# Kernel tuning notes

Hardware: AMD Instinct MI355X
Metric: run time of the kernel (lower is better)

Reference implementation:

```python
import jax, jax.numpy as jnp
import numpy as np

D_MODEL = 1024
N_HEADS = 16
D_K = D_MODEL // N_HEADS  # 64


def setup_inputs() -> dict:
    key = jax.random.key(0)
    ks = jax.random.split(key, 12)
    B, S = 2, 2048
    inp = {
        "query": jax.random.normal(ks[0], (B, S, D_MODEL), jnp.float32),
        "key": jax.random.normal(ks[1], (B, S, D_MODEL), jnp.float32),
        "value": jax.random.normal(ks[2], (B, S, D_MODEL), jnp.float32),
        "mask": jnp.ones((B, 1, S, S), jnp.int32),
    }
    sc = 1.0 / np.sqrt(D_MODEL)
    inp["Wq"] = jax.random.normal(ks[3], (D_MODEL, D_MODEL), jnp.float32) * sc
    inp["bq"] = jnp.zeros((D_MODEL,), jnp.float32)
    inp["Wk"] = jax.random.normal(ks[4], (D_MODEL, D_MODEL), jnp.float32) * sc
    inp["bk"] = jnp.zeros((D_MODEL,), jnp.float32)
    inp["Wv"] = jax.random.normal(ks[5], (D_MODEL, D_MODEL), jnp.float32) * sc
    inp["bv"] = jnp.zeros((D_MODEL,), jnp.float32)
    inp["Wo"] = jax.random.normal(ks[6], (D_MODEL, D_MODEL), jnp.float32) * sc
    inp["bo"] = jnp.zeros((D_MODEL,), jnp.float32)
    return inp


def reference(query, key, value, mask, Wq, bq, Wk, bk, Wv, bv, Wo, bo):
    B, Sq, _ = query.shape
    H, dk = N_HEADS, D_K
    # linear projections, split heads: (B,S,D) -> (B,H,S,dk)
    def split_heads(x):
        return x.reshape(B, -1, H, dk).transpose(0, 2, 1, 3)
    Q = split_heads(query @ Wq.T + bq)
    K = split_heads(key @ Wk.T + bk)
    V = split_heads(value @ Wv.T + bv)
    scale = 1.0 / jnp.sqrt(jnp.asarray(dk, jnp.float32))
    scores = jnp.einsum('bhqd,bhkd->bhqk', Q, K) * scale
    scores = jnp.where(mask == 0, jnp.asarray(-1e9, scores.dtype), scores)
    attn = jax.nn.softmax(scores, axis=-1)  # (B,H,Sq,Sk)
    out = jnp.einsum('bhqk,bhkd->bhqd', attn, V)
    out = out.transpose(0, 2, 1, 3).reshape(B, Sq, D_MODEL)
    out = out @ Wo.T + bo
    return out, attn
```

## Files before the change

kernel.cpp:

```cpp
#include <hip/hip_runtime.h>
#include <cstdint>
#include <cstddef>

#define DEV __device__ __forceinline__

typedef float f32x4 __attribute__((ext_vector_type(4)));
typedef __bf16 bf16x8 __attribute__((ext_vector_type(8)));
typedef unsigned short u16x8 __attribute__((ext_vector_type(8)));

static constexpr int D = 1024, H = 16, DK = 64, S = 2048, B = 2;
static constexpr int M_TOT = B * S;
static constexpr size_t OUT0 = (size_t)M_TOT * D;

DEV unsigned short f2bf(float f) {
  unsigned x = __builtin_bit_cast(unsigned, f);
  unsigned r = (x + 0x7fffu + ((x >> 16) & 1u)) >> 16;
  return (unsigned short)r;
}

DEV float bf2f(unsigned short u) {
  return __builtin_bit_cast(float, (unsigned)u << 16);
}

DEV f32x4 mfma_bf16(bf16x8 a, bf16x8 b, f32x4 c) {
  return __builtin_amdgcn_mfma_f32_16x16x32_bf16(a, b, c, 0, 0, 0);
}

DEV bf16x8 bc(u16x8 u) { return __builtin_bit_cast(bf16x8, u); }

template <int MODE, bool ABF16, bool WBF16>
DEV void proj_body(unsigned short* As, unsigned short* Bs, const void* Aptr,
                   const void* W, const float* bias, void* dst) {
  constexpr int BM = 128, BK = 32, LDT = 40;
  const int tid = threadIdx.x;
  const int lane = tid & 63, wave = tid >> 6;
  const int wrow = wave >> 1, wcol = wave & 1;
  const int l15 = lane & 15, kg = lane >> 4;
  const int m0 = blockIdx.y * BM, n0 = blockIdx.x * BM;
  const int srow = tid >> 1, scb = (tid & 1) * 16;

  f32x4 acc[4][4] = {};

  for (int kt = 0; kt < D; kt += BK) {
    {
      u16x8 t0, t1;
      if constexpr (ABF16) {
        const unsigned short* ap =
            (const unsigned short*)Aptr + (size_t)(m0 + srow) * D + kt + scb;
        t0 = *(const u16x8*)ap;
        t1 = *(const u16x8*)(ap + 8);
      } else {
        const float* ap = (const float*)Aptr + (size_t)(m0 + srow) * D + kt + scb;
        float4 v0 = *(const float4*)(ap + 0);
        float4 v1 = *(const float4*)(ap + 4);
        float4 v2 = *(const float4*)(ap + 8);
        float4 v3 = *(const float4*)(ap + 12);
        t0[0] = f2bf(v0.x); t0[1] = f2bf(v0.y); t0[2] = f2bf(v0.z); t0[3] = f2bf(v0.w);
        t0[4] = f2bf(v1.x); t0[5] = f2bf(v1.y); t0[6] = f2bf(v1.z); t0[7] = f2bf(v1.w);
        t1[0] = f2bf(v2.x); t1[1] = f2bf(v2.y); t1[2] = f2bf(v2.z); t1[3] = f2bf(v2.w);
        t1[4] = f2bf(v3.x); t1[5] = f2bf(v3.y); t1[6] = f2bf(v3.z); t1[7] = f2bf(v3.w);
      }
      *(u16x8*)&As[srow * LDT + scb] = t0;
      *(u16x8*)&As[srow * LDT + scb + 8] = t1;

      u16x8 s0, s1;
      if constexpr (WBF16) {
        const unsigned short* wp =
            (const unsigned short*)W + (size_t)(n0 + srow) * D + kt + scb;
        s0 = *(const u16x8*)wp;
        s1 = *(const u16x8*)(wp + 8);
      } else {
        const float* bp = (const float*)W + (size_t)(n0 + srow) * D + kt + scb;
        float4 w0 = *(const float4*)(bp + 0);
        float4 w1 = *(const float4*)(bp + 4);
        float4 w2 = *(const float4*)(bp + 8);
        float4 w3 = *(const float4*)(bp + 12);
        s0[0] = f2bf(w0.x); s0[1] = f2bf(w0.y); s0[2] = f2bf(w0.z); s0[3] = f2bf(w0.w);
        s0[4] = f2bf(w1.x); s0[5] = f2bf(w1.y); s0[6] = f2bf(w1.z); s0[7] = f2bf(w1.w);
        s1[0] = f2bf(w2.x); s1[1] = f2bf(w2.y); s1[2] = f2bf(w2.z); s1[3] = f2bf(w2.w);
        s1[4] = f2bf(w3.x); s1[5] = f2bf(w3.y); s1[6] = f2bf(w3.z); s1[7] = f2bf(w3.w);
      }
      *(u16x8*)&Bs[srow * LDT + scb] = s0;
      *(u16x8*)&Bs[srow * LDT + scb + 8] = s1;
    }
    __syncthreads();

    bf16x8 a[4], b[4];
#pragma unroll
    for (int i = 0; i < 4; i++)
      a[i] = bc(*(const u16x8*)&As[(wrow * 64 + i * 16 + l15) * LDT + kg * 8]);
#pragma unroll
    for (int i = 0; i < 4; i++)
      b[i] = bc(*(const u16x8*)&Bs[(wcol * 64 + i * 16 + l15) * LDT + kg * 8]);
#pragma unroll
    for (int mi = 0; mi < 4; mi++)
#pragma unroll
      for (int ni = 0; ni < 4; ni++) acc[mi][ni] = mfma_bf16(a[mi], b[ni], acc[mi][ni]);
    __syncthreads();
  }

#pragma unroll
  for (int mi = 0; mi < 4; mi++) {
#pragma unroll
    for (int ni = 0; ni < 4; ni++) {
      const int n = n0 + wcol * 64 + ni * 16 + l15;
      const float bval = bias[n];
#pragma unroll
      for (int r = 0; r < 4; r++) {
        const int m = m0 + wrow * 64 + mi * 16 + kg * 4 + r;
        float v = acc[mi][ni][r] + bval;
        if constexpr (MODE == 0) v *= 0.125f;
        if constexpr (MODE == 0 || MODE == 1) {
          const int b_ = m >> 11, s = m & (S - 1), h = n >> 6, d_ = n & (DK - 1);
          ((unsigned short*)dst)[(((size_t)(b_ * H + h)) * S + s) * DK + d_] = f2bf(v);
        } else if constexpr (MODE == 2) {
          const int b_ = m >> 11, s = m & (S - 1), h = n >> 6, d_ = n & (DK - 1);
          ((unsigned short*)dst)[(((size_t)(b_ * H + h)) * DK + d_) * S + s] = f2bf(v);
        } else {
          ((float*)dst)[(size_t)m * D + n] = v;
        }
      }
    }
  }
}

struct PrepArgs {
  const float* A[3];
  const float* W[3];
  const float* bias[3];
  unsigned short* dst[3];
  const int* mask;
  unsigned long long* bits;
  const float* Wo;
  unsigned short* WoBf;
};

__global__ __launch_bounds__(256) void qkv_prep(PrepArgs pa) {
  __shared__ __align__(16) unsigned short As[128 * 40];
  __shared__ __align__(16) unsigned short Bs[128 * 40];
  const int z = blockIdx.z;
  if (z == 0) {
    proj_body<0, false, false>(As, Bs, pa.A[0], pa.W[0], pa.bias[0], pa.dst[0]);
  } else if (z == 1) {
    proj_body<1, false, false>(As, Bs, pa.A[1], pa.W[1], pa.bias[1], pa.dst[1]);
  } else if (z == 2) {
    proj_body<2, false, false>(As, Bs, pa.A[2], pa.W[2], pa.bias[2], pa.dst[2]);
  } else {
    const int gid = blockIdx.y * 8 + blockIdx.x;
    const int tid = threadIdx.x, lane = tid & 63;
    const int base = gid * 512;
    for (int w = base + (tid >> 6); w < base + 512; w += 4) {
      int m = __builtin_nontemporal_load(pa.mask + (size_t)w * 64 + lane);
      unsigned long long bal = __ballot(m != 0);
      if (lane == 0) pa.bits[w] = bal;
    }
    {
      const size_t i0 = (size_t)gid * 4096 + (size_t)tid * 16;
      float4 v0 = *(const float4*)(pa.Wo + i0);
      float4 v1 = *(const float4*)(pa.Wo + i0 + 4);
      float4 v2 = *(const float4*)(pa.Wo + i0 + 8);
      float4 v3 = *(const float4*)(pa.Wo + i0 + 12);
      u16x8 t0, t1;
      t0[0] = f2bf(v0.x); t0[1] = f2bf(v0.y); t0[2] = f2bf(v0.z); t0[3] = f2bf(v0.w);
      t0[4] = f2bf(v1.x); t0[5] = f2bf(v1.y); t0[6] = f2bf(v1.z); t0[7] = f2bf(v1.w);
      t1[0] = f2bf(v2.x); t1[1] = f2bf(v2.y); t1[2] = f2bf(v2.z); t1[3] = f2bf(v2.w);
      t1[4] = f2bf(v3.x); t1[5] = f2bf(v3.y); t1[6] = f2bf(v3.z); t1[7] = f2bf(v3.w);
      *(u16x8*)(pa.WoBf + i0) = t0;
      *(u16x8*)(pa.WoBf + i0 + 8) = t1;
    }
  }
}

__global__ __launch_bounds__(256) void out_proj(const unsigned short* __restrict__ ctx,
                                                const unsigned short* __restrict__ WoBf,
                                                const float* __restrict__ bo,
                                                float* __restrict__ out) {
  __shared__ __align__(16) unsigned short As[128 * 40];
  __shared__ __align__(16) unsigned short Bs[128 * 40];
  proj_body<3, true, true>(As, Bs, ctx, WoBf, bo, out);
}

__global__ __launch_bounds__(1024, 4) void attn_kernel(
    const unsigned short* __restrict__ Qb, const unsigned short* __restrict__ Kb,
    const unsigned short* __restrict__ Vt, const unsigned* __restrict__ bits32,
    float* __restrict__ attn_out, unsigned short* __restrict__ ctx) {
  constexpr int QB = 32, SROW = 2056;
  __shared__ __align__(16) unsigned short es[QB * SROW];
  __shared__ unsigned mlds[QB * 64];
  __shared__ float rsum[16 * QB];
  __shared__ float rinv_s[QB];
  __shared__ float opart[4 * QB * 17];

  const int wg = blockIdx.x;
  const int qblk = wg & 63, h = (wg >> 6) & 15, b_ = wg >> 10;
  const int bh = b_ * H + h;
  const int qb0 = qblk * QB;
  const int tid = threadIdx.x, lane = tid & 63, wave = tid >> 6;
  const int l15 = lane & 15, kg = lane >> 4;
  const int rowq = kg * 4;
  constexpr float LOG2E = 1.44269504088896340736f;

#pragma unroll
  for (int i = 0; i < 2; i++) {
    const int idx = tid + i * 1024;
    mlds[idx] = bits32[((size_t)b_ * S + qb0 + (idx >> 6)) * 64 + (idx & 63)];
  }

  const unsigned short* qbase = Qb + ((size_t)bh * S + qb0) * DK;
  bf16x8 aq[2][2];
#pragma unroll
  for (int rg = 0; rg < 2; rg++)
#pragma unroll
    for (int hf = 0; hf < 2; hf++)
      aq[rg][hf] =
          bc(*(const u16x8*)(qbase + (size_t)(rg * 16 + l15) * DK + hf * 32 + kg * 8));
  __syncthreads();

  float sum[2][4] = {};
#pragma unroll 2
  for (int i = 0; i < 8; i++) {
    const int t = wave * 8 + i;
    const unsigned short* krow = Kb + ((size_t)bh * S + t * 16 + l15) * DK;
    bf16x8 b0 = bc(*(const u16x8*)(krow + kg * 8));
    bf16x8 b1 = bc(*(const u16x8*)(krow + 32 + kg * 8));
    const unsigned shift = (unsigned)((t & 1) * 16 + l15);
#pragma unroll
    for (int rg = 0; rg < 2; rg++) {
      f32x4 c = {0.f, 0.f, 0.f, 0.f};
      c = mfma_bf16(aq[rg][0], b0, c);
      c = mfma_bf16(aq[rg][1], b1, c);
#pragma unroll
      for (int r = 0; r < 4; r++) {
        const int row = rg * 16 + rowq + r;
        const unsigned w = mlds[row * 64 + (t >> 1)];
        const float e = ((w >> shift) & 1u) ? exp2f(c[r] * LOG2E) : 0.f;
        sum[rg][r] += e;
        es[row * SROW + t * 16 + l15] = f2bf(e);
      }
    }
  }

#pragma unroll
  for (int rg = 0; rg < 2; rg++)
#pragma unroll
    for (int r = 0; r < 4; r++) {
      float s = sum[rg][r];
      s += __shfl_xor(s, 1);
      s += __shfl_xor(s, 2);
      s += __shfl_xor(s, 4);
      s += __shfl_xor(s, 8);
      if (l15 == 0) rsum[wave * QB + rg * 16 + rowq + r] = s;
    }
  __syncthreads();
  if (tid < QB) {
    float t2 = 0.f;
#pragma unroll
    for (int w = 0; w < 16; w++) t2 += rsum[w * QB + tid];
    rinv_s[tid] = 1.f / t2;
  }
  __syncthreads();

  f32x4 o[2] = {};
  if (wave < 8) {
#pragma unroll
    for (int rr = 0; rr < 4; rr++) {
      const int row = wave * 4 + rr;
      const float ri = rinv_s[row];
      float* dstp = attn_out + ((size_t)bh * S + qb0 + row) * S;
#pragma unroll
      for (int j = 0; j < 4; j++) {
        u16x8 u = *(const u16x8*)&es[row * SROW + j * 512 + lane * 8];
        f32x4 lo, hi;
        lo[0] = bf2f(u[0]) * ri; lo[1] = bf2f(u[1]) * ri;
        lo[2] = bf2f(u[2]) * ri; lo[3] = bf2f(u[3]) * ri;
        hi[0] = bf2f(u[4]) * ri; hi[1] = bf2f(u[5]) * ri;
        hi[2] = bf2f(u[6]) * ri; hi[3] = bf2f(u[7]) * ri;
        __builtin_nontemporal_store(lo, (f32x4*)(dstp + j * 512 + lane * 8));
        __builtin_nontemporal_store(hi, (f32x4*)(dstp + j * 512 + lane * 8 + 4));
      }
    }
  } else {
    const int pw = wave - 8, dg = pw & 3, kh = pw >> 2;
    const unsigned short* vrow =
        Vt + ((size_t)bh * DK + dg * 16 + l15) * S + kh * 1024;
    const unsigned short* ebase = es + kh * 1024 + kg * 8;
#pragma unroll 2
    for (int ks = 0; ks < 32; ks++) {
      bf16x8 bv = bc(*(const u16x8*)(vrow + ks * 32 + kg * 8));
#pragma unroll
      for (int rg = 0; rg < 2; rg++) {
        bf16x8 af = bc(*(const u16x8*)&ebase[(size_t)(rg * 16 + l15) * SROW + ks * 32]);
        o[rg] = mfma_bf16(af, bv, o[rg]);
      }
    }
    if (kh == 1) {
#pragma unroll
      for (int rg = 0; rg < 2; rg++)
#pragma unroll
        for (int r = 0; r < 4; r++)
          opart[dg * (QB * 17) + (rg * 16 + rowq + r) * 17 + l15] = o[rg][r];
    }
  }
  __syncthreads();

  if (wave >= 8 && ((wave - 8) >> 2) == 0) {
    const int dg = (wave - 8) & 3;
#pragma unroll
    for (int rg = 0; rg < 2; rg++)
#pragma unroll
      for (int r = 0; r < 4; r++) {
        const int row = rg * 16 + rowq + r;
        const float v =
            (o[rg][r] + opart[dg * (QB * 17) + row * 17 + l15]) * rinv_s[row];
        ctx[((size_t)(b_ * S + qb0 + row)) * D + h * DK + dg * 16 + l15] = f2bf(v);
      }
  }
}

extern "C" void kernel_launch(void* const* d_in, const int* in_sizes, int n_in,
                              void* d_out, int out_size, void* d_ws, size_t ws_size,
                              hipStream_t stream) {
  const float* query = (const float*)d_in[0];
  const float* key   = (const float*)d_in[1];
  const float* value = (const float*)d_in[2];
  const int*   mask  = (const int*)d_in[3];
  const float* Wq = (const float*)d_in[4];
  const float* bq = (const float*)d_in[5];
  const float* Wk = (const float*)d_in[6];
  const float* bk = (const float*)d_in[7];
  const float* Wv = (const float*)d_in[8];
  const float* bv = (const float*)d_in[9];
  const float* Wo = (const float*)d_in[10];
  const float* bo = (const float*)d_in[11];

  float* out_p = (float*)d_out;
  float* attn_p = (float*)d_out + OUT0;

  size_t off = 0;
  auto carve = [&](size_t bytes) {
    void* p = (char*)d_ws + off;
    off += (bytes + 255) & ~(size_t)255;
    return p;
  };
  const size_t headed = (size_t)B * H * S * DK * sizeof(unsigned short);
  unsigned short* Qb = (unsigned short*)carve(headed);
  unsigned short* Kb = (unsigned short*)carve(headed);
  unsigned short* Vt = (unsigned short*)carve(headed);
  unsigned short* ctx = (unsigned short*)carve((size_t)M_TOT * D * sizeof(unsigned short));
  unsigned long long* bits = (unsigned long long*)carve((size_t)B * S * S / 8);
  unsigned short* WoBf = (unsigned short*)carve((size_t)D * D * sizeof(unsigned short));

  PrepArgs pa;
  pa.A[0] = query; pa.A[1] = key; pa.A[2] = value;
  pa.W[0] = Wq; pa.W[1] = Wk; pa.W[2] = Wv;
  pa.bias[0] = bq; pa.bias[1] = bk; pa.bias[2] = bv;
  pa.dst[0] = Qb; pa.dst[1] = Kb; pa.dst[2] = Vt;
  pa.mask = mask; pa.bits = bits; pa.Wo = Wo; pa.WoBf = WoBf;

  qkv_prep<<<dim3(8, 32, 4), 256, 0, stream>>>(pa);

  attn_kernel<<<B * H * (S / 32), 1024, 0, stream>>>(Qb, Kb, Vt, (const unsigned*)bits,
                                                     attn_p, ctx);

  out_proj<<<dim3(8, 32), 256, 0, stream>>>(ctx, WoBf, bo, out_p);
}
```

Measured before the change: 420.3 us.

## Recompute scores in second pass to shrink LDS and stream normalized probabilities

The attention kernel moves from 1024 to 512 threads and from a full 32x2048 bf16 score buffer in shared memory to a two-pass scheme. Pass one computes only row sums. Pass two recomputes QK^T and exp per 256-column strip, writes the normalized probabilities straight to global memory, and double-buffers them in a small LDS tile for the PV MFMA. This cuts LDS use a lot, allowing more resident workgroups, and spreads the attn stores across all waves. The cost is twice the QK^T and exp work, plus scalar (non-vectorized) nontemporal stores of attn and a barrier per strip.

```diff
diff --git a/kernel.cpp b/kernel.cpp
--- a/kernel.cpp
+++ b/kernel.cpp
@@ -180,14 +180,15 @@
   proj_body<3, true, true>(As, Bs, ctx, WoBf, bo, out);
 }
 
-__global__ __launch_bounds__(1024, 4) void attn_kernel(
+__global__ __launch_bounds__(512, 4) void attn_kernel(
     const unsigned short* __restrict__ Qb, const unsigned short* __restrict__ Kb,
     const unsigned short* __restrict__ Vt, const unsigned* __restrict__ bits32,
     float* __restrict__ attn_out, unsigned short* __restrict__ ctx) {
-  constexpr int QB = 32, SROW = 2056;
-  __shared__ __align__(16) unsigned short es[QB * SROW];
+  constexpr int QB = 32;
+  constexpr int PROW = 264;
+  __shared__ __align__(16) unsigned short pbuf[2][QB * PROW];
   __shared__ unsigned mlds[QB * 64];
-  __shared__ float rsum[16 * QB];
+  __shared__ float rsum[8 * QB];
   __shared__ float rinv_s[QB];
   __shared__ float opart[4 * QB * 17];
 
@@ -201,8 +202,8 @@
   constexpr float LOG2E = 1.44269504088896340736f;
 
 #pragma unroll
-  for (int i = 0; i < 2; i++) {
-    const int idx = tid + i * 1024;
+  for (int i = 0; i < 4; i++) {
+    const int idx = tid + i * 512;
     mlds[idx] = bits32[((size_t)b_ * S + qb0 + (idx >> 6)) * 64 + (idx & 63)];
   }
 
@@ -218,8 +219,8 @@
 
   float sum[2][4] = {};
 #pragma unroll 2
-  for (int i = 0; i < 8; i++) {
-    const int t = wave * 8 + i;
+  for (int i = 0; i < 16; i++) {
+    const int t = wave * 16 + i;
     const unsigned short* krow = Kb + ((size_t)bh * S + t * 16 + l15) * DK;
     bf16x8 b0 = bc(*(const u16x8*)(krow + kg * 8));
     bf16x8 b1 = bc(*(const u16x8*)(krow + 32 + kg * 8));
@@ -233,9 +234,7 @@
       for (int r = 0; r < 4; r++) {
         const int row = rg * 16 + rowq + r;
         const unsigned w = mlds[row * 64 + (t >> 1)];
-        const float e = ((w >> shift) & 1u) ? exp2f(c[r] * LOG2E) : 0.f;
-        sum[rg][r] += e;
-        es[row * SROW + t * 16 + l15] = f2bf(e);
+        sum[rg][r] += ((w >> shift) & 1u) ? exp2f(c[r] * LOG2E) : 0.f;
       }
     }
   }
@@ -255,63 +254,77 @@
   if (tid < QB) {
     float t2 = 0.f;
 #pragma unroll
-    for (int w = 0; w < 16; w++) t2 += rsum[w * QB + tid];
+    for (int w = 0; w < 8; w++) t2 += rsum[w * QB + tid];
     rinv_s[tid] = 1.f / t2;
   }
   __syncthreads();
 
+  float ri[2][4];
+#pragma unroll
+  for (int rg = 0; rg < 2; rg++)
+#pragma unroll
+    for (int r = 0; r < 4; r++) ri[rg][r] = rinv_s[rg * 16 + rowq + r];
+
+  const int dg = wave & 3, ksub = wave >> 2;
+  const unsigned short* vrow = Vt + ((size_t)bh * DK + dg * 16 + l15) * S + ksub * 128;
+  float* abase = attn_out + ((size_t)bh * S + qb0) * S;
   f32x4 o[2] = {};
-  if (wave < 8) {
-#pragma unroll
-    for (int rr = 0; rr < 4; rr++) {
-      const int row = wave * 4 + rr;
-      const float ri = rinv_s[row];
-      float* dstp = attn_out + ((size_t)bh * S + qb0 + row) * S;
-#pragma unroll
-      for (int j = 0; j < 4; j++) {
-        u16x8 u = *(const u16x8*)&es[row * SROW + j * 512 + lane * 8];
-        f32x4 lo, hi;
-        lo[0] = bf2f(u[0]) * ri; lo[1] = bf2f(u[1]) * ri;
-        lo[2] = bf2f(u[2]) * ri; lo[3] = bf2f(u[3]) * ri;
-        hi[0] = bf2f(u[4]) * ri; hi[1] = bf2f(u[5]) * ri;
-        hi[2] = bf2f(u[6]) * ri; hi[3] = bf2f(u[7]) * ri;
-        __builtin_nontemporal_store(lo, (f32x4*)(dstp + j * 512 + lane * 8));
-        __builtin_nontemporal_store(hi, (f32x4*)(dstp + j * 512 + lane * 8 + 4));
-      }
-    }
-  } else {
-    const int pw = wave - 8, dg = pw & 3, kh = pw >> 2;
-    const unsigned short* vrow =
-        Vt + ((size_t)bh * DK + dg * 16 + l15) * S + kh * 1024;
-    const unsigned short* ebase = es + kh * 1024 + kg * 8;
-#pragma unroll 2
-    for (int ks = 0; ks < 32; ks++) {
-      bf16x8 bv = bc(*(const u16x8*)(vrow + ks * 32 + kg * 8));
+
+  for (int sb = 0; sb < 8; sb++) {
+    unsigned short* pb = pbuf[sb & 1];
+#pragma unroll
+    for (int j = 0; j < 2; j++) {
+      const int t = sb * 16 + wave * 2 + j;
+      const unsigned short* krow = Kb + ((size_t)bh * S + t * 16 + l15) * DK;
+      bf16x8 b0 = bc(*(const u16x8*)(krow + kg * 8));
+      bf16x8 b1 = bc(*(const u16x8*)(krow + 32 + kg * 8));
+      const unsigned shift = (unsigned)((t & 1) * 16 + l15);
+      const int lc = (wave * 2 + j) * 16 + l15;
 #pragma unroll
       for (int rg = 0; rg < 2; rg++) {
-        bf16x8 af = bc(*(const u16x8*)&ebase[(size_t)(rg * 16 + l15) * SROW + ks * 32]);
+        f32x4 c = {0.f, 0.f, 0.f, 0.f};
+        c = mfma_bf16(aq[rg][0], b0, c);
+        c = mfma_bf16(aq[rg][1], b1, c);
+#pragma unroll
+        for (int r = 0; r < 4; r++) {
+          const int row = rg * 16 + rowq + r;
+          const unsigned w = mlds[row * 64 + (t >> 1)];
+          const float e = ((w >> shift) & 1u) ? exp2f(c[r] * LOG2E) : 0.f;
+          const float p = e * ri[rg][r];
+          __builtin_nontemporal_store(p, abase + (size_t)row * S + t * 16 + l15);
+          pb[row * PROW + lc] = f2bf(p);
+        }
+      }
+    }
+    __syncthreads();
+    const unsigned short* vv = vrow + sb * 256;
+#pragma unroll
+    for (int ks = 0; ks < 4; ks++) {
+      bf16x8 bv = bc(*(const u16x8*)(vv + ks * 32 + kg * 8));
+#pragma unroll
+      for (int rg = 0; rg < 2; rg++) {
+        bf16x8 af = bc(
+            *(const u16x8*)&pb[(rg * 16 + l15) * PROW + ksub * 128 + ks * 32 + kg * 8]);
         o[rg] = mfma_bf16(af, bv, o[rg]);
       }
     }
-    if (kh == 1) {
-#pragma unroll
-      for (int rg = 0; rg < 2; rg++)
-#pragma unroll
-        for (int r = 0; r < 4; r++)
-          opart[dg * (QB * 17) + (rg * 16 + rowq + r) * 17 + l15] = o[rg][r];
-    }
+  }
+
+  if (ksub == 1) {
+#pragma unroll
+    for (int rg = 0; rg < 2; rg++)
+#pragma unroll
+      for (int r = 0; r < 4; r++)
+        opart[dg * (QB * 17) + (rg * 16 + rowq + r) * 17 + l15] = o[rg][r];
   }
   __syncthreads();
-
-  if (wave >= 8 && ((wave - 8) >> 2) == 0) {
-    const int dg = (wave - 8) & 3;
+  if (ksub == 0) {
 #pragma unroll
     for (int rg = 0; rg < 2; rg++)
 #pragma unroll
       for (int r = 0; r < 4; r++) {
         const int row = rg * 16 + rowq + r;
-        const float v =
-            (o[rg][r] + opart[dg * (QB * 17) + row * 17 + l15]) * rinv_s[row];
+        const float v = o[rg][r] + opart[dg * (QB * 17) + row * 17 + l15];
         ctx[((size_t)(b_ * S + qb0 + row)) * D + h * DK + dg * 16 + l15] = f2bf(v);
       }
   }
@@ -359,8 +372,8 @@
 
   qkv_prep<<<dim3(8, 32, 4), 256, 0, stream>>>(pa);
 
-  attn_kernel<<<B * H * (S / 32), 1024, 0, stream>>>(Qb, Kb, Vt, (const unsigned*)bits,
-                                                     attn_p, ctx);
+  attn_kernel<<<B * H * (S / 32), 512, 0, stream>>>(Qb, Kb, Vt, (const unsigned*)bits,
+                                                    attn_p, ctx);
 
   out_proj<<<dim3(8, 32), 256, 0, stream>>>(ctx, WoBf, bo, out_p);
 }
```

Measured after the change: 366.6 us. -12.8%, faster.
